# Performance work log

Measured on AMD Instinct MI355X. Metric: run time of the kernel, lower is better.

## Reference

```python
import jax, jax.numpy as jnp
import numpy as np

MARGIN = 0.5
BETA, GAMMA = 0.5, 0.2   # hard-coded in _get_triplet_selection_function
NUM_ANCHORS = 30          # hard-coded in select()
EPS_COS = 1e-8

B, C, D = 320, 80, 128


def setup_inputs() -> dict:
    key = jax.random.key(0)
    k1, k2, k3 = jax.random.split(key, 3)
    label = jax.random.randint(k1, (B, C), 0, 2).astype(jnp.int32)
    source = jax.random.normal(k2, (B, D), dtype=jnp.float32)
    target = jax.random.normal(k3, (B, D), dtype=jnp.float32)
    return {"label": label, "source": source, "target": target}


def _cos_distance(src, tgt):
    # F.cosine_similarity(src.unsqueeze(1), tgt, dim=-1): [B, B] sim matrix
    ns = jnp.linalg.norm(src, axis=-1)          # [B]
    nt = jnp.linalg.norm(tgt, axis=-1)          # [B]
    sim = (src @ tgt.T) / jnp.maximum(ns[:, None] * nt[None, :], EPS_COS)
    return jnp.clip(1.0 - sim, 0.0)


def _label_distances(labels_f):
    dot = labels_f @ labels_f.T                 # [B, B]
    sn = jnp.sqrt(jnp.diagonal(dot))            # [B]
    norms = sn[None, :] * sn[:, None]
    return 1.0 - jnp.minimum(1.0, dot / norms)


def _base_mask(b):
    ine = ~jnp.eye(b, dtype=bool)               # indices_not_equal
    # (a!=p) & (a!=n) & (p!=n)  ->  [B, B, B]
    return ine[:, :, None] & ine[:, None, :] & ine[None, :, :]


def _anchor_mask(fd, num_anchors):
    # select_diverse_anchors: pick the num_anchors anchors with the largest
    # mean feature distance to all other samples (most "diverse").
    diversity = jnp.mean(fd, axis=1)            # [B]
    _, idx = jax.lax.top_k(diversity, num_anchors)
    m = jnp.zeros((fd.shape[0],), dtype=bool).at[idx].set(True)
    return m[:, None, None]                     # broadcastable over (a, p, n)


def _triplet_mask(ld, beta, gamma):
    # select_triplets_smartly: (a, p) must be label-similar (dist <= gamma)
    # and (a, n) must be label-dissimilar (dist >= beta).
    pos = ld <= gamma                           # [B, B] over (a, p)
    neg = ld >= beta                            # [B, B] over (a, n)
    return pos[:, :, None] & neg[:, None, :]


def reference(label, source, target):
    fd = _cos_distance(source, target)                       # [B, B]
    ld = _label_distances(label.astype(jnp.float32))         # [B, B]
    mask = (_base_mask(fd.shape[0])
            & _anchor_mask(fd, NUM_ANCHORS)
            & _triplet_mask(ld, BETA, GAMMA))                # [B, B, B]
    # triplet_loss[a,p,n] = fd[a,p] - fd[a,n] + margin
    tl = fd[:, :, None] - fd[:, None, :] + MARGIN
    tl = jnp.clip(jnp.where(mask, tl, 0.0), 0.0)
    num_pos = jnp.sum(mask.astype(jnp.float32))
    return jnp.sum(tl) / (num_pos + 1e-4)
```

## Files before the change

### kernel.cpp

```cpp
#include <hip/hip_runtime.h>
#include <cstdint>

namespace {

constexpr int NB = 320;
constexpr int ND = 128;
constexpr int NC = 80;
constexpr int NANCH = 30;
constexpr int NW = 5;

constexpr size_t OFF_DIV  = 0;
constexpr size_t OFF_ASUM = 1280;
constexpr size_t OFF_ACNT = 3840;
constexpr size_t OFF_PACK = 5120;
constexpr size_t OFF_TGTT = 10240;

__global__ __launch_bounds__(256) void k_prep(
    const float* __restrict__ tgt,
    const int* __restrict__ label,
    float2* __restrict__ tgtT2,
    unsigned long long* __restrict__ packed)
{
    const int tid = threadIdx.x;
    const int w = tid >> 6, lane = tid & 63;
    const int r0 = blockIdx.x * 64;

    __shared__ float tile[64][133];

    if (w == 0) {
        const int r = r0 + lane;
        const int4* lp = reinterpret_cast<const int4*>(label + r * NC);
        unsigned long long j0 = 0, j1 = 0;
#pragma unroll
        for (int q = 0; q < 16; ++q) {
            int4 v = lp[q];
            j0 |= (unsigned long long)(v.x != 0) << (4 * q + 0);
            j0 |= (unsigned long long)(v.y != 0) << (4 * q + 1);
            j0 |= (unsigned long long)(v.z != 0) << (4 * q + 2);
            j0 |= (unsigned long long)(v.w != 0) << (4 * q + 3);
        }
#pragma unroll
        for (int q = 16; q < 20; ++q) {
            int4 v = lp[q];
            const int b = 4 * (q - 16);
            j1 |= (unsigned long long)(v.x != 0) << (b + 0);
            j1 |= (unsigned long long)(v.y != 0) << (b + 1);
            j1 |= (unsigned long long)(v.z != 0) << (b + 2);
            j1 |= (unsigned long long)(v.w != 0) << (b + 3);
        }
        packed[2 * r]     = j0;
        packed[2 * r + 1] = j1;
    }

#pragma unroll
    for (int it = 0; it < 8; ++it) {
        const int f4 = it * 256 + tid;
        float4 v = reinterpret_cast<const float4*>(tgt)[r0 * (ND / 4) + f4];
        const int r = f4 >> 5, d4 = (f4 & 31) << 2;
        tile[r][d4 + 0] = v.x; tile[r][d4 + 1] = v.y;
        tile[r][d4 + 2] = v.z; tile[r][d4 + 3] = v.w;
    }
    __syncthreads();

#pragma unroll
    for (int it = 0; it < 16; ++it) {
        const int d2 = it * 4 + w;
        float2 o;
        o.x = tile[lane][2 * d2 + 0];
        o.y = tile[lane][2 * d2 + 1];
        tgtT2[d2 * NB + r0 + lane] = o;
    }
}

__global__ __launch_bounds__(256) void k_main(
    const float* __restrict__ src,
    const float2* __restrict__ tgtT2,
    const unsigned long long* __restrict__ packed,
    float* __restrict__ divr,
    double* __restrict__ asum,
    int* __restrict__ acnt)
{
    const int a = blockIdx.x;
    const int tid = threadIdx.x;
    const int w = tid >> 6, lane = tid & 63;

    __shared__ float sa[ND];
    __shared__ float snsa;
    __shared__ float red[256];
    __shared__ unsigned long long pk[2 * NB];
    __shared__ float fdrow[NB];
    __shared__ unsigned long long pmask[NW], nmask[NW];
    __shared__ double wsum[4];

    if (tid < ND) sa[tid] = src[a * ND + tid];
    if (w == 0) {
        float s0 = src[a * ND + lane];
        float s1 = src[a * ND + lane + 64];
        float v = s0 * s0 + s1 * s1;
        for (int off = 32; off > 0; off >>= 1) v += __shfl_down(v, off);
        if (lane == 0) snsa = sqrtf(v);
    }
    for (int q = tid; q < 2 * NB; q += 256) pk[q] = packed[q];
    __syncthreads();

    const unsigned long long a0 = pk[2 * a], a1 = pk[2 * a + 1];
    const float nsa = snsa;

    float acc = 0.f;
#pragma unroll
    for (int it = 0; it < 2; ++it) {
        const int j = tid + 256 * it;
        if (j < NB) {
            float dot = 0.f, tn = 0.f;
#pragma unroll
            for (int d = 0; d < ND / 4; ++d) {
                float2 u = tgtT2[(2 * d + 0) * NB + j];
                float2 v = tgtT2[(2 * d + 1) * NB + j];
                dot += sa[4 * d + 0] * u.x + sa[4 * d + 1] * u.y +
                       sa[4 * d + 2] * v.x + sa[4 * d + 3] * v.y;
                tn += u.x * u.x + u.y * u.y + v.x * v.x + v.y * v.y;
            }
            float sim = dot / fmaxf(nsa * sqrtf(tn), 1e-8f);
            float f = fmaxf(1.0f - sim, 0.0f);
            fdrow[j] = f;
            acc += f;
        }
    }

    red[tid] = acc;
    __syncthreads();
    for (int st = 128; st > 0; st >>= 1) {
        if (tid < st) red[tid] += red[tid + st];
        __syncthreads();
    }
    if (tid == 0) divr[a] = red[0] / (float)NB;

    const float sna = sqrtf((float)(__popcll(a0) + __popcll(a1)));
#pragma unroll
    for (int it = 0; it < 2; ++it) {
        const int jj = tid + 256 * it;
        if (jj < NB) {
            const unsigned long long j0 = pk[2 * jj], j1 = pk[2 * jj + 1];
            const float snj = sqrtf((float)(__popcll(j0) + __popcll(j1)));
            const float denom = sna * snj;
            const float dotf = (float)(__popcll(a0 & j0) + __popcll(a1 & j1));
            const float ld = 1.0f - fminf(1.0f, dotf / denom);
            const bool valid = (jj != a) && (denom > 0.f);
            unsigned long long pb = __ballot(valid && (ld <= 0.2f));
            unsigned long long nb = __ballot(valid && (ld >= 0.5f));
            if (lane == 0) { pmask[jj >> 6] = pb; nmask[jj >> 6] = nb; }
        }
    }
    __syncthreads();

    double s = 0.0;
#pragma unroll
    for (int it = 0; it < 2; ++it) {
        const int jj = tid + 256 * it;
        if (jj < NB && ((nmask[jj >> 6] >> (jj & 63)) & 1ull)) {
            const float fn = fdrow[jj];
#pragma unroll
            for (int wd = 0; wd < NW; ++wd) {
                unsigned long long m = pmask[wd];
                while (m) {
                    const int b = __builtin_ctzll(m);
                    m &= m - 1;
                    float v = fdrow[wd * 64 + b] - fn + 0.5f;
                    if (v > 0.f) s += (double)v;
                }
            }
        }
    }
    for (int off = 32; off > 0; off >>= 1) s += __shfl_down(s, off);
    if (lane == 0) wsum[w] = s;
    __syncthreads();
    if (tid == 0) {
        int P = 0, N = 0;
#pragma unroll
        for (int wd = 0; wd < NW; ++wd) {
            P += __popcll(pmask[wd]);
            N += __popcll(nmask[wd]);
        }
        asum[a] = wsum[0] + wsum[1] + wsum[2] + wsum[3];
        acnt[a] = P * N;
    }
}

__global__ __launch_bounds__(320) void k_final(
    const float* __restrict__ divr,
    const double* __restrict__ asum,
    const int* __restrict__ acnt,
    float* __restrict__ out)
{
    const int tid = threadIdx.x;
    __shared__ float dv[NB];
    __shared__ int alist[NANCH];
    __shared__ double sl[NANCH];
    __shared__ int cl[NANCH];

    dv[tid] = divr[tid];
    __syncthreads();

    const float ve = dv[tid];
    int rank = 0;
#pragma unroll 8
    for (int j = 0; j < NB; ++j) {
        float vj = dv[j];
        rank += (vj > ve) || (vj == ve && j < tid);
    }
    if (rank < NANCH) alist[rank] = tid;
    __syncthreads();

    if (tid < NANCH) {
        sl[tid] = asum[alist[tid]];
        cl[tid] = acnt[alist[tid]];
    }
    __syncthreads();
    if (tid == 0) {
        double S = 0.0;
        long long C = 0;
        for (int r = 0; r < NANCH; ++r) { S += sl[r]; C += cl[r]; }
        out[0] = (float)(S / ((double)C + 1e-4));
    }
}

}

extern "C" void kernel_launch(void* const* d_in, const int* in_sizes, int n_in,
                              void* d_out, int out_size, void* d_ws, size_t ws_size,
                              hipStream_t stream) {
    const int* label = (const int*)d_in[0];
    const float* src = (const float*)d_in[1];
    const float* tgt = (const float*)d_in[2];

    char* ws = (char*)d_ws;
    float* divr  = (float*)(ws + OFF_DIV);
    double* asum = (double*)(ws + OFF_ASUM);
    int* acnt    = (int*)(ws + OFF_ACNT);
    unsigned long long* packed = (unsigned long long*)(ws + OFF_PACK);
    float2* tgtT2 = (float2*)(ws + OFF_TGTT);

    k_prep <<<5, 256, 0, stream>>>(tgt, label, tgtT2, packed);
    k_main <<<NB, 256, 0, stream>>>(src, tgtT2, packed, divr, asum, acnt);
    k_final<<<1, 320, 0, stream>>>(divr, asum, acnt, (float*)d_out);
}
```

Measured before the change: 31.34 us.

## Fold final top-k reduction into main kernel via last-block atomic counter

```diff
diff --git a/kernel.cpp b/kernel.cpp
--- a/kernel.cpp
+++ b/kernel.cpp
@@ -14,18 +14,22 @@
 constexpr size_t OFF_ACNT = 3840;
 constexpr size_t OFF_PACK = 5120;
 constexpr size_t OFF_TGTT = 10240;
+constexpr size_t OFF_CTR  = 174080;
 
 __global__ __launch_bounds__(256) void k_prep(
     const float* __restrict__ tgt,
     const int* __restrict__ label,
     float2* __restrict__ tgtT2,
-    unsigned long long* __restrict__ packed)
+    unsigned long long* __restrict__ packed,
+    unsigned int* __restrict__ ctr)
 {
     const int tid = threadIdx.x;
     const int w = tid >> 6, lane = tid & 63;
     const int r0 = blockIdx.x * 64;
 
     __shared__ float tile[64][133];
+
+    if (blockIdx.x == 0 && tid == 0) *ctr = 0;
 
     if (w == 0) {
         const int r = r0 + lane;
@@ -72,13 +76,15 @@
     }
 }
 
-__global__ __launch_bounds__(256) void k_main(
+__global__ __launch_bounds__(512) void k_main(
     const float* __restrict__ src,
     const float2* __restrict__ tgtT2,
     const unsigned long long* __restrict__ packed,
     float* __restrict__ divr,
     double* __restrict__ asum,
-    int* __restrict__ acnt)
+    int* __restrict__ acnt,
+    unsigned int* __restrict__ ctr,
+    float* __restrict__ out)
 {
     const int a = blockIdx.x;
     const int tid = threadIdx.x;
@@ -91,6 +97,11 @@
     __shared__ float fdrow[NB];
     __shared__ unsigned long long pmask[NW], nmask[NW];
     __shared__ double wsum[4];
+    __shared__ int isLastS;
+    __shared__ float dv[NB];
+    __shared__ int alist[NANCH];
+    __shared__ double sl[NANCH];
+    __shared__ int cl[NANCH];
 
     if (tid < ND) sa[tid] = src[a * ND + tid];
     if (w == 0) {
@@ -100,34 +111,29 @@
         for (int off = 32; off > 0; off >>= 1) v += __shfl_down(v, off);
         if (lane == 0) snsa = sqrtf(v);
     }
-    for (int q = tid; q < 2 * NB; q += 256) pk[q] = packed[q];
+    for (int q = tid; q < 2 * NB; q += 512) pk[q] = packed[q];
     __syncthreads();
 
     const unsigned long long a0 = pk[2 * a], a1 = pk[2 * a + 1];
     const float nsa = snsa;
 
-    float acc = 0.f;
-#pragma unroll
-    for (int it = 0; it < 2; ++it) {
-        const int j = tid + 256 * it;
-        if (j < NB) {
-            float dot = 0.f, tn = 0.f;
-#pragma unroll
-            for (int d = 0; d < ND / 4; ++d) {
-                float2 u = tgtT2[(2 * d + 0) * NB + j];
-                float2 v = tgtT2[(2 * d + 1) * NB + j];
-                dot += sa[4 * d + 0] * u.x + sa[4 * d + 1] * u.y +
-                       sa[4 * d + 2] * v.x + sa[4 * d + 3] * v.y;
-                tn += u.x * u.x + u.y * u.y + v.x * v.x + v.y * v.y;
-            }
-            float sim = dot / fmaxf(nsa * sqrtf(tn), 1e-8f);
-            float f = fmaxf(1.0f - sim, 0.0f);
-            fdrow[j] = f;
-            acc += f;
-        }
-    }
-
-    red[tid] = acc;
+    if (tid < NB) {
+        float dot = 0.f, tn = 0.f;
+#pragma unroll
+        for (int d = 0; d < ND / 4; ++d) {
+            float2 u = tgtT2[(2 * d + 0) * NB + tid];
+            float2 v = tgtT2[(2 * d + 1) * NB + tid];
+            dot += sa[4 * d + 0] * u.x + sa[4 * d + 1] * u.y +
+                   sa[4 * d + 2] * v.x + sa[4 * d + 3] * v.y;
+            tn += u.x * u.x + u.y * u.y + v.x * v.x + v.y * v.y;
+        }
+        float sim = dot / fmaxf(nsa * sqrtf(tn), 1e-8f);
+        fdrow[tid] = fmaxf(1.0f - sim, 0.0f);
+    }
+    __syncthreads();
+
+    if (tid < 256)
+        red[tid] = (tid < 64) ? fdrow[tid] + fdrow[tid + 256] : fdrow[tid];
     __syncthreads();
     for (int st = 128; st > 0; st >>= 1) {
         if (tid < st) red[tid] += red[tid + st];
@@ -136,43 +142,41 @@
     if (tid == 0) divr[a] = red[0] / (float)NB;
 
     const float sna = sqrtf((float)(__popcll(a0) + __popcll(a1)));
-#pragma unroll
-    for (int it = 0; it < 2; ++it) {
-        const int jj = tid + 256 * it;
-        if (jj < NB) {
-            const unsigned long long j0 = pk[2 * jj], j1 = pk[2 * jj + 1];
-            const float snj = sqrtf((float)(__popcll(j0) + __popcll(j1)));
-            const float denom = sna * snj;
-            const float dotf = (float)(__popcll(a0 & j0) + __popcll(a1 & j1));
-            const float ld = 1.0f - fminf(1.0f, dotf / denom);
-            const bool valid = (jj != a) && (denom > 0.f);
-            unsigned long long pb = __ballot(valid && (ld <= 0.2f));
-            unsigned long long nb = __ballot(valid && (ld >= 0.5f));
-            if (lane == 0) { pmask[jj >> 6] = pb; nmask[jj >> 6] = nb; }
-        }
+    if (tid < NB) {
+        const unsigned long long j0 = pk[2 * tid], j1 = pk[2 * tid + 1];
+        const float snj = sqrtf((float)(__popcll(j0) + __popcll(j1)));
+        const float denom = sna * snj;
+        const float dotf = (float)(__popcll(a0 & j0) + __popcll(a1 & j1));
+        const float ld = 1.0f - fminf(1.0f, dotf / denom);
+        const bool valid = (tid != a) && (denom > 0.f);
+        unsigned long long pb = __ballot(valid && (ld <= 0.2f));
+        unsigned long long nb = __ballot(valid && (ld >= 0.5f));
+        if (lane == 0) { pmask[w] = pb; nmask[w] = nb; }
     }
     __syncthreads();
 
     double s = 0.0;
-#pragma unroll
-    for (int it = 0; it < 2; ++it) {
-        const int jj = tid + 256 * it;
-        if (jj < NB && ((nmask[jj >> 6] >> (jj & 63)) & 1ull)) {
-            const float fn = fdrow[jj];
-#pragma unroll
-            for (int wd = 0; wd < NW; ++wd) {
-                unsigned long long m = pmask[wd];
-                while (m) {
-                    const int b = __builtin_ctzll(m);
-                    m &= m - 1;
-                    float v = fdrow[wd * 64 + b] - fn + 0.5f;
-                    if (v > 0.f) s += (double)v;
+    if (w < 4) {
+#pragma unroll
+        for (int it = 0; it < 2; ++it) {
+            const int jj = tid + 256 * it;
+            if (jj < NB && ((nmask[jj >> 6] >> (jj & 63)) & 1ull)) {
+                const float fn = fdrow[jj];
+#pragma unroll
+                for (int wd = 0; wd < NW; ++wd) {
+                    unsigned long long m = pmask[wd];
+                    while (m) {
+                        const int b = __builtin_ctzll(m);
+                        m &= m - 1;
+                        float v = fdrow[wd * 64 + b] - fn + 0.5f;
+                        if (v > 0.f) s += (double)v;
+                    }
                 }
             }
         }
-    }
-    for (int off = 32; off > 0; off >>= 1) s += __shfl_down(s, off);
-    if (lane == 0) wsum[w] = s;
+        for (int off = 32; off > 0; off >>= 1) s += __shfl_down(s, off);
+        if (lane == 0) wsum[w] = s;
+    }
     __syncthreads();
     if (tid == 0) {
         int P = 0, N = 0;
@@ -183,34 +187,26 @@
         }
         asum[a] = wsum[0] + wsum[1] + wsum[2] + wsum[3];
         acnt[a] = P * N;
-    }
-}
-
-__global__ __launch_bounds__(320) void k_final(
-    const float* __restrict__ divr,
-    const double* __restrict__ asum,
-    const int* __restrict__ acnt,
-    float* __restrict__ out)
-{
-    const int tid = threadIdx.x;
-    __shared__ float dv[NB];
-    __shared__ int alist[NANCH];
-    __shared__ double sl[NANCH];
-    __shared__ int cl[NANCH];
-
-    dv[tid] = divr[tid];
-    __syncthreads();
-
-    const float ve = dv[tid];
-    int rank = 0;
+        __threadfence();
+        isLastS = (atomicAdd(ctr, 1u) == (unsigned)(NB - 1));
+    }
+    __syncthreads();
+    if (!isLastS) return;
+    __threadfence();
+
+    if (tid < NB) dv[tid] = divr[tid];
+    __syncthreads();
+    if (tid < NB) {
+        const float ve = dv[tid];
+        int rank = 0;
 #pragma unroll 8
-    for (int j = 0; j < NB; ++j) {
-        float vj = dv[j];
-        rank += (vj > ve) || (vj == ve && j < tid);
-    }
-    if (rank < NANCH) alist[rank] = tid;
-    __syncthreads();
-
+        for (int j = 0; j < NB; ++j) {
+            float vj = dv[j];
+            rank += (vj > ve) || (vj == ve && j < tid);
+        }
+        if (rank < NANCH) alist[rank] = tid;
+    }
+    __syncthreads();
     if (tid < NANCH) {
         sl[tid] = asum[alist[tid]];
         cl[tid] = acnt[alist[tid]];
@@ -239,8 +235,9 @@
     int* acnt    = (int*)(ws + OFF_ACNT);
     unsigned long long* packed = (unsigned long long*)(ws + OFF_PACK);
     float2* tgtT2 = (float2*)(ws + OFF_TGTT);
-
-    k_prep <<<5, 256, 0, stream>>>(tgt, label, tgtT2, packed);
-    k_main <<<NB, 256, 0, stream>>>(src, tgtT2, packed, divr, asum, acnt);
-    k_final<<<1, 320, 0, stream>>>(divr, asum, acnt, (float*)d_out);
-}
+    unsigned int* ctr = (unsigned int*)(ws + OFF_CTR);
+
+    k_prep<<<5, 256, 0, stream>>>(tgt, label, tgtT2, packed, ctr);
+    k_main<<<NB, 512, 0, stream>>>(src, tgtT2, packed, divr, asum, acnt, ctr,
+                                   (float*)d_out);
+}
```

After: 35.23 us. +12.4%, slower.
